# Kernel optimization log

Measured on AMD Instinct MI355X. Metric: run time of the kernel, lower is better.

Reference implementation:

```python
import jax, jax.numpy as jnp
import numpy as np

FSIZE = 5
PAD = FSIZE // 2


def _conv(mosaick, filts):
    # mosaick [B,1,H,W], filts [f,f,K] -> responses [B,K,H,W].
    # Cross-correlation with edge-clamped boundary (Halide clamp semantics).
    x = jnp.pad(mosaick, ((0, 0), (0, 0), (PAD, PAD), (PAD, PAD)), mode='edge')
    k = jnp.transpose(filts, (2, 0, 1))[:, None, :, :]  # [K,1,f,f] OIHW
    return jax.lax.conv_general_dilated(
        x, k, window_strides=(1, 1), padding='VALID',
        dimension_numbers=('NCHW', 'OIHW', 'NCHW'))


def setup_inputs() -> dict:
    key = jax.random.key(0)
    k1, k2, k3 = jax.random.split(key, 3)
    B, H, W, K, f = 16, 512, 512, 8, FSIZE
    std = 1.0 / (f * f)  # matches normal_(0, 1/(fsize*fsize))
    return {
        'mosaick': jax.random.normal(k1, (B, 1, H, W), dtype=jnp.float32),
        'sel_filts': jax.random.normal(k2, (f, f, K), dtype=jnp.float32) * std,
        'green_filts': jax.random.normal(k3, (f, f, K), dtype=jnp.float32) * std,
    }


def reference(mosaick, sel_filts, green_filts):
    # Per-pixel soft filter selection over K candidate green-interpolation filters.
    sel = _conv(mosaick, sel_filts)      # [B,K,H,W] selection scores
    grn = _conv(mosaick, green_filts)    # [B,K,H,W] candidate green estimates
    w = jax.nn.softmax(sel, axis=1)      # softmax over filter bank
    interp = jnp.sum(w * grn, axis=1, keepdims=True)  # [B,1,H,W]
    # GRBG Bayer: green where row parity == col parity; copy known greens.
    H, W = mosaick.shape[-2], mosaick.shape[-1]
    yy = jnp.arange(H)[:, None]
    xx = jnp.arange(W)[None, :]
    is_green = (yy % 2) == (xx % 2)      # [H,W] bool
    # Output green channel only (module returns output[:, 1:2, ...]).
    return jnp.where(is_green, mosaick, interp)
```

## Files before the change

### kernel.cpp

```cpp
#include <hip/hip_runtime.h>


typedef float f32x16 __attribute__((ext_vector_type(16)));
typedef short s16x8  __attribute__((ext_vector_type(8)));

#define HH 512
#define WW 512
#define TW 64
#define TH 16
#define RS 80
#define NROW 20
#define NEL 72

__device__ __forceinline__ unsigned short bf16rne(float x) {
    unsigned u = __float_as_uint(x);
    u += 0x7fffu + ((u >> 16) & 1u);
    return (unsigned short)(u >> 16);
}
__device__ __forceinline__ int pk2(float hi, float lo) {
    return (int)((((unsigned)bf16rne(hi)) << 16) | (unsigned)bf16rne(lo));
}
__device__ __forceinline__ float hi16(int v) { return __uint_as_float(((unsigned)v) & 0xffff0000u); }
__device__ __forceinline__ float lo16(int v) { return __uint_as_float(((unsigned)v) << 16); }

__global__ void build_frags_kernel(const float* __restrict__ sf,
                                   const float* __restrict__ gf,
                                   short* __restrict__ ws)
{
    const int lane = threadIdx.x;
    const int mm   = lane & 31;
    const int h    = (lane >> 5) & 1;
    const int c    = mm >> 1;
    const bool tg  = mm & 1;
    const bool chok = mm < 16;
    const float* fb = tg ? gf : sf;

    s16x8 A[6];
#pragma unroll
    for (int f = 0; f < 6; ++f)
#pragma unroll
        for (int j = 0; j < 8; ++j) A[f][j] = 0;

#pragma unroll
    for (int j = 0; j < 8; ++j) {
        const int dx0 = j - 1;
        if (dx0 >= 0 && dx0 < 5 && chok) {
            A[0][j] = (short)bf16rne(fb[((h)     * 5 + dx0) * 8 + c]);
            A[1][j] = (short)bf16rne(fb[((2 + h) * 5 + dx0) * 8 + c]);
            if (h == 0)
                A[2][j] = (short)bf16rne(fb[(4 * 5 + dx0) * 8 + c]);
        }
        const int dx1 = j;
        if (dx1 < 5 && chok) {
            if (h == 1)
                A[3][j] = (short)bf16rne(fb[(0 * 5 + dx1) * 8 + c]);
            A[4][j] = (short)bf16rne(fb[((1 + h) * 5 + dx1) * 8 + c]);
            A[5][j] = (short)bf16rne(fb[((3 + h) * 5 + dx1) * 8 + c]);
        }
    }
    s16x8* dst = (s16x8*)(ws + lane * 48);
#pragma unroll
    for (int f = 0; f < 6; ++f) dst[f] = A[f];
}

__global__ __launch_bounds__(256) void demosaick_kernel(
    const float* __restrict__ mos,
    const short* __restrict__ frg,
    float* __restrict__ out)
{
    __shared__ alignas(16) unsigned short tileS[NROW * RS];

    const int tid   = threadIdx.x;
    const int bx    = blockIdx.x;
    const int by    = blockIdx.y;
    const int bimg  = blockIdx.z;
    const int tileX = bx * TW;
    const int tileY = by * TH;
    const float* img = mos + (size_t)bimg * HH * WW;

    const bool interior = (bx >= 1) && (bx <= 6) && (by >= 1) && (by <= 30);
    if (interior) {
        if (tid < 180) {
            int r = tid / 9, s = tid - 9 * r;
            const float2* src = (const float2*)(img + (size_t)(tileY - 2 + r) * WW
                                                + (tileX - 2 + 8 * s));
            float2 v0 = src[0], v1 = src[1], v2 = src[2], v3 = src[3];
            int4 d;
            d.x = pk2(v0.y, v0.x);
            d.y = pk2(v1.y, v1.x);
            d.z = pk2(v2.y, v2.x);
            d.w = pk2(v3.y, v3.x);
            *(int4*)&tileS[r * RS + 8 * s] = d;
        }
    } else {
        for (int i = tid; i < NROW * NEL; i += 256) {
            int r = i / NEL, e = i - NEL * r;
            int gy = min(max(tileY - 2 + r, 0), HH - 1);
            int gx = min(max(tileX - 2 + e, 0), WW - 1);
            tileS[r * RS + e] = bf16rne(img[(size_t)gy * WW + gx]);
        }
    }

    const int lane = tid & 63;
    const int w    = tid >> 6;
    const int n    = lane & 31;
    const int h    = lane >> 5;

    const s16x8* wsf = (const s16x8*)(frg + lane * 48);
    const s16x8 Aa0 = wsf[0], Ab0 = wsf[1], Ac0 = wsf[2];
    const s16x8 Aa1 = wsf[3], Ab1 = wsf[4], Ac1 = wsf[5];

    __syncthreads();

    const int* tb = (const int*)tileS;
    float* outp = out + (size_t)bimg * HH * WW;

#pragma unroll
    for (int pp = 0; pp < 2; ++pp) {
        const int Rl = 4 * w + 2 * pp;
        const int y  = tileY + Rl;
        const int ia = (Rl + h) * 40 + n;

        union { int4 v; s16x8 s; } Ba, Bb, Bc;
        Ba.v.x = tb[ia];       Ba.v.y = tb[ia + 1];
        Ba.v.z = tb[ia + 2];   Ba.v.w = tb[ia + 3];
        Bb.v.x = tb[ia + 80];  Bb.v.y = tb[ia + 81];
        Bb.v.z = tb[ia + 82];  Bb.v.w = tb[ia + 83];
        Bc.v.x = tb[ia + 160]; Bc.v.y = tb[ia + 161];
        Bc.v.z = tb[ia + 162]; Bc.v.w = tb[ia + 163];

        f32x16 acc = (f32x16)(0.f);
        acc = __builtin_amdgcn_mfma_f32_32x32x16_bf16(Aa0, Ba.s, acc, 0, 0, 0);
        acc = __builtin_amdgcn_mfma_f32_32x32x16_bf16(Ab0, Bb.s, acc, 0, 0, 0);
        acc = __builtin_amdgcn_mfma_f32_32x32x16_bf16(Ac0, Bc.s, acc, 0, 0, 0);
        {
            float den = 0.f, num = 0.f;
#pragma unroll
            for (int j = 0; j < 4; ++j) {
                float e = __expf(acc[2 * j]);
                den += e;
                num = fmaf(e, acc[2 * j + 1], num);
            }
            int nd  = pk2(num, den);
            int nd2 = __shfl_xor(nd, 32);
            num += hi16(nd2);
            den += lo16(nd2);
            const float interp = num * __builtin_amdgcn_rcpf(den);
            if (h == 0) {
                const int x0 = tileX + 2 * n;
                const float green = img[(size_t)y * WW + x0];
                float2 st; st.x = green; st.y = interp;
                *(float2*)(outp + (size_t)y * WW + x0) = st;
            }
        }

        f32x16 acc2 = (f32x16)(0.f);
        acc2 = __builtin_amdgcn_mfma_f32_32x32x16_bf16(Aa1, Ba.s, acc2, 0, 0, 0);
        acc2 = __builtin_amdgcn_mfma_f32_32x32x16_bf16(Ab1, Bb.s, acc2, 0, 0, 0);
        acc2 = __builtin_amdgcn_mfma_f32_32x32x16_bf16(Ac1, Bc.s, acc2, 0, 0, 0);
        {
            float den = 0.f, num = 0.f;
#pragma unroll
            for (int j = 0; j < 4; ++j) {
                float e = __expf(acc2[2 * j]);
                den += e;
                num = fmaf(e, acc2[2 * j + 1], num);
            }
            int nd  = pk2(num, den);
            int nd2 = __shfl_xor(nd, 32);
            num += hi16(nd2);
            den += lo16(nd2);
            const float interp = num * __builtin_amdgcn_rcpf(den);
            if (h == 0) {
                const int x0 = tileX + 2 * n;
                const float green = img[(size_t)(y + 1) * WW + x0 + 1];
                float2 st; st.x = interp; st.y = green;
                *(float2*)(outp + (size_t)(y + 1) * WW + x0) = st;
            }
        }
    }
}

extern "C" void kernel_launch(void* const* d_in, const int* in_sizes, int n_in,
                              void* d_out, int out_size, void* d_ws, size_t ws_size,
                              hipStream_t stream) {
    const float* mos = (const float*)d_in[0];
    const float* sf  = (const float*)d_in[1];
    const float* gf  = (const float*)d_in[2];
    float* out = (float*)d_out;
    short* ws  = (short*)d_ws;

    const int B = in_sizes[0] / (HH * WW);

    build_frags_kernel<<<1, 64, 0, stream>>>(sf, gf, ws);

    dim3 grid(WW / TW, HH / TH, B);
    dim3 block(256);
    demosaick_kernel<<<grid, block, 0, stream>>>(mos, (const short*)ws, out);
}
```

Measured before the change: 85.46 us.

## Share LDS B-fragments across row pairs and balance epilogue across half-waves

Loads four B fragments once per wave and reuses the overlapping ones across both row pairs, so LDS reads drop from six fragments to four. The twelve MFMAs are interleaved across four independent accumulators to hide MFMA latency. The shuffle reduction is rearranged so both half-waves produce outputs, removing the idle h==1 lanes in the epilogue and halving the number of shuffles. The filter fragment load is also hoisted ahead of the tile fill. The cost is higher register pressure from holding four 16-wide accumulators at once.

```diff
diff --git a/kernel.cpp b/kernel.cpp
--- a/kernel.cpp
+++ b/kernel.cpp
@@ -77,6 +77,15 @@
     const int tileX = bx * TW;
     const int tileY = by * TH;
     const float* img = mos + (size_t)bimg * HH * WW;
+
+    const int lane = tid & 63;
+    const int w    = tid >> 6;
+    const int n    = lane & 31;
+    const int h    = lane >> 5;
+
+    const s16x8* wsf = (const s16x8*)(frg + lane * 48);
+    const s16x8 Aa0 = wsf[0], Ab0 = wsf[1], Ac0 = wsf[2];
+    const s16x8 Aa1 = wsf[3], Ab1 = wsf[4], Ac1 = wsf[5];
 
     const bool interior = (bx >= 1) && (bx <= 6) && (by >= 1) && (by <= 30);
     if (interior) {
@@ -100,85 +109,79 @@
             tileS[r * RS + e] = bf16rne(img[(size_t)gy * WW + gx]);
         }
     }
-
-    const int lane = tid & 63;
-    const int w    = tid >> 6;
-    const int n    = lane & 31;
-    const int h    = lane >> 5;
-
-    const s16x8* wsf = (const s16x8*)(frg + lane * 48);
-    const s16x8 Aa0 = wsf[0], Ab0 = wsf[1], Ac0 = wsf[2];
-    const s16x8 Aa1 = wsf[3], Ab1 = wsf[4], Ac1 = wsf[5];
-
     __syncthreads();
 
     const int* tb = (const int*)tileS;
+
+    union { int4 v; s16x8 s; } B[4];
+#pragma unroll
+    for (int r = 0; r < 4; ++r) {
+        const int ia = (4 * w + 2 * r + h) * 40 + n;
+        B[r].v.x = tb[ia];     B[r].v.y = tb[ia + 1];
+        B[r].v.z = tb[ia + 2]; B[r].v.w = tb[ia + 3];
+    }
+
+    f32x16 a00 = (f32x16)(0.f), a01 = (f32x16)(0.f);
+    f32x16 a10 = (f32x16)(0.f), a11 = (f32x16)(0.f);
+    a00 = __builtin_amdgcn_mfma_f32_32x32x16_bf16(Aa0, B[0].s, a00, 0, 0, 0);
+    a01 = __builtin_amdgcn_mfma_f32_32x32x16_bf16(Aa1, B[0].s, a01, 0, 0, 0);
+    a10 = __builtin_amdgcn_mfma_f32_32x32x16_bf16(Aa0, B[1].s, a10, 0, 0, 0);
+    a11 = __builtin_amdgcn_mfma_f32_32x32x16_bf16(Aa1, B[1].s, a11, 0, 0, 0);
+    a00 = __builtin_amdgcn_mfma_f32_32x32x16_bf16(Ab0, B[1].s, a00, 0, 0, 0);
+    a01 = __builtin_amdgcn_mfma_f32_32x32x16_bf16(Ab1, B[1].s, a01, 0, 0, 0);
+    a10 = __builtin_amdgcn_mfma_f32_32x32x16_bf16(Ab0, B[2].s, a10, 0, 0, 0);
+    a11 = __builtin_amdgcn_mfma_f32_32x32x16_bf16(Ab1, B[2].s, a11, 0, 0, 0);
+    a00 = __builtin_amdgcn_mfma_f32_32x32x16_bf16(Ac0, B[2].s, a00, 0, 0, 0);
+    a01 = __builtin_amdgcn_mfma_f32_32x32x16_bf16(Ac1, B[2].s, a01, 0, 0, 0);
+    a10 = __builtin_amdgcn_mfma_f32_32x32x16_bf16(Ac0, B[3].s, a10, 0, 0, 0);
+    a11 = __builtin_amdgcn_mfma_f32_32x32x16_bf16(Ac1, B[3].s, a11, 0, 0, 0);
+
+    float nums[4], dens[4];
+    {
+        const f32x16* av[4] = { &a00, &a01, &a10, &a11 };
+#pragma unroll
+        for (int r = 0; r < 4; ++r) {
+            float den = 0.f, num = 0.f;
+            const f32x16& a = *av[r];
+#pragma unroll
+            for (int j = 0; j < 4; ++j) {
+                float e = __expf(a[2 * j]);
+                den += e;
+                num = fmaf(e, a[2 * j + 1], num);
+            }
+            nums[r] = num; dens[r] = den;
+        }
+    }
+
+    const int nd0 = pk2(nums[0], dens[0]);
+    const int nd1 = pk2(nums[1], dens[1]);
+    const int nd2 = pk2(nums[2], dens[2]);
+    const int nd3 = pk2(nums[3], dens[3]);
+
+    const int send0 = h ? nd0 : nd2;
+    const int send1 = h ? nd1 : nd3;
+    const int rec0  = __shfl_xor(send0, 32);
+    const int rec1  = __shfl_xor(send1, 32);
+    const int mine0 = h ? nd2 : nd0;
+    const int mine1 = h ? nd3 : nd1;
+
+    const float numA = hi16(mine0) + hi16(rec0);
+    const float denA = lo16(mine0) + lo16(rec0);
+    const float numB = hi16(mine1) + hi16(rec1);
+    const float denB = lo16(mine1) + lo16(rec1);
+    const float interpA = numA * __builtin_amdgcn_rcpf(denA);
+    const float interpB = numB * __builtin_amdgcn_rcpf(denB);
+
     float* outp = out + (size_t)bimg * HH * WW;
-
-#pragma unroll
-    for (int pp = 0; pp < 2; ++pp) {
-        const int Rl = 4 * w + 2 * pp;
-        const int y  = tileY + Rl;
-        const int ia = (Rl + h) * 40 + n;
-
-        union { int4 v; s16x8 s; } Ba, Bb, Bc;
-        Ba.v.x = tb[ia];       Ba.v.y = tb[ia + 1];
-        Ba.v.z = tb[ia + 2];   Ba.v.w = tb[ia + 3];
-        Bb.v.x = tb[ia + 80];  Bb.v.y = tb[ia + 81];
-        Bb.v.z = tb[ia + 82];  Bb.v.w = tb[ia + 83];
-        Bc.v.x = tb[ia + 160]; Bc.v.y = tb[ia + 161];
-        Bc.v.z = tb[ia + 162]; Bc.v.w = tb[ia + 163];
-
-        f32x16 acc = (f32x16)(0.f);
-        acc = __builtin_amdgcn_mfma_f32_32x32x16_bf16(Aa0, Ba.s, acc, 0, 0, 0);
-        acc = __builtin_amdgcn_mfma_f32_32x32x16_bf16(Ab0, Bb.s, acc, 0, 0, 0);
-        acc = __builtin_amdgcn_mfma_f32_32x32x16_bf16(Ac0, Bc.s, acc, 0, 0, 0);
-        {
-            float den = 0.f, num = 0.f;
-#pragma unroll
-            for (int j = 0; j < 4; ++j) {
-                float e = __expf(acc[2 * j]);
-                den += e;
-                num = fmaf(e, acc[2 * j + 1], num);
-            }
-            int nd  = pk2(num, den);
-            int nd2 = __shfl_xor(nd, 32);
-            num += hi16(nd2);
-            den += lo16(nd2);
-            const float interp = num * __builtin_amdgcn_rcpf(den);
-            if (h == 0) {
-                const int x0 = tileX + 2 * n;
-                const float green = img[(size_t)y * WW + x0];
-                float2 st; st.x = green; st.y = interp;
-                *(float2*)(outp + (size_t)y * WW + x0) = st;
-            }
-        }
-
-        f32x16 acc2 = (f32x16)(0.f);
-        acc2 = __builtin_amdgcn_mfma_f32_32x32x16_bf16(Aa1, Ba.s, acc2, 0, 0, 0);
-        acc2 = __builtin_amdgcn_mfma_f32_32x32x16_bf16(Ab1, Bb.s, acc2, 0, 0, 0);
-        acc2 = __builtin_amdgcn_mfma_f32_32x32x16_bf16(Ac1, Bc.s, acc2, 0, 0, 0);
-        {
-            float den = 0.f, num = 0.f;
-#pragma unroll
-            for (int j = 0; j < 4; ++j) {
-                float e = __expf(acc2[2 * j]);
-                den += e;
-                num = fmaf(e, acc2[2 * j + 1], num);
-            }
-            int nd  = pk2(num, den);
-            int nd2 = __shfl_xor(nd, 32);
-            num += hi16(nd2);
-            den += lo16(nd2);
-            const float interp = num * __builtin_amdgcn_rcpf(den);
-            if (h == 0) {
-                const int x0 = tileX + 2 * n;
-                const float green = img[(size_t)(y + 1) * WW + x0 + 1];
-                float2 st; st.x = interp; st.y = green;
-                *(float2*)(outp + (size_t)(y + 1) * WW + x0) = st;
-            }
-        }
-    }
+    const int y  = tileY + 4 * w + 2 * h;
+    const int x0 = tileX + 2 * n;
+
+    const float greenA = img[(size_t)y * WW + x0];
+    const float greenB = img[(size_t)(y + 1) * WW + x0 + 1];
+    float2 stA; stA.x = greenA;  stA.y = interpA;
+    float2 stB; stB.x = interpB; stB.y = greenB;
+    *(float2*)(outp + (size_t)y * WW + x0)       = stA;
+    *(float2*)(outp + (size_t)(y + 1) * WW + x0) = stB;
 }
 
 extern "C" void kernel_launch(void* const* d_in, const int* in_sizes, int n_in,
```

After: 86.77 us. Within noise of the previous version (+1.5%).
